# Kernel tuning notes

Hardware: AMD Instinct MI355X
Metric: run time of the kernel (lower is better)

Reference implementation:

```python
import jax, jax.numpy as jnp
import numpy as np

B, S, C, L, H = 128, 8, 120, 469, 64


def setup_inputs() -> dict:
    key = jax.random.key(0)
    kx, kk, kq, kv = jax.random.split(key, 4)
    scale = 1.0 / np.sqrt(L)
    x = jax.random.normal(kx, (B, S, C, L), dtype=jnp.float32)
    # nn.Linear(L, H, bias=False): y = x @ W^T with W:[H,L]; store as [L,H] so y = x @ W
    Wk = jax.random.normal(kk, (L, H), dtype=jnp.float32) * scale
    Wq = jax.random.normal(kq, (L, H), dtype=jnp.float32) * scale
    Wv = jax.random.normal(kv, (L, H), dtype=jnp.float32) * scale
    return {"x": x, "Wk": Wk, "Wq": Wq, "Wv": Wv}


def reference(x, Wk, Wq, Wv):
    b, s, c, l = x.shape
    h = Wk.shape[-1]
    # torch: x.view(S_, B, C_, L_) -- a raw reshape, not a permute
    xs = x.reshape(s, b, c, l)
    k = xs @ Wk  # (s, b, c, h)
    q = xs @ Wq
    v = xs @ Wv
    wei = jnp.einsum('sbch,sbdh->sbcd', q, k) * (h ** -0.5)
    wei = jax.nn.softmax(wei, axis=-1)  # dropout = identity in eval
    out = jnp.einsum('sbcd,sbdh->sbch', wei, v)  # (s, b, c, h)
    # torch: matrices.view(B, S_, C_, head_size) -- raw reshape again
    return out.reshape(b, s, c, h)
```

## Files before the change

kernel.cpp:

```cpp
#include <hip/hip_runtime.h>
#include <hip/hip_bf16.h>

typedef __attribute__((ext_vector_type(8))) short bf16x8;
typedef __attribute__((ext_vector_type(4))) float f32x4;
typedef float f32x4u __attribute__((ext_vector_type(4), aligned(4)));
typedef __attribute__((ext_vector_type(4))) short short4v;
typedef unsigned short ushort_t;

#define CC 120
#define LL 469
#define HH 64

constexpr int NBATCH = 1024;
constexpr int KSTEPS = 15;

constexpr int WB_SHORTS   = 8192;
constexpr int SMEM_BYTES  = 49152;
constexpr int WIMG_SHORTS = KSTEPS * WB_SHORTS;
constexpr int WIMG_BYTES  = WIMG_SHORTS * 2;

__device__ __forceinline__ ushort_t f2bf(float f) {
  __hip_bfloat16 h = __float2bfloat16(f);
  return __builtin_bit_cast(ushort_t, h);
}

__device__ __forceinline__ void gload_lds16(const void* g, void* l) {
  __builtin_amdgcn_global_load_lds(
      (const __attribute__((address_space(1))) unsigned int*)g,
      (__attribute__((address_space(3))) unsigned int*)l, 16, 0, 0);
}

__device__ __forceinline__ char* sptr(char* base, int row, int stride, int byteoff) {
  return base + row * stride + (byteoff ^ ((row & 7) << 4));
}

__global__ void prep_w(const float* __restrict__ Wk, const float* __restrict__ Wq,
                       const float* __restrict__ Wv, ushort_t* __restrict__ wimg) {
  int idx = blockIdx.x * 256 + threadIdx.x;
  int t = idx / WB_SHORTS;
  int r = idx % WB_SHORTS;
  int col = r / 40, kk = r % 40;
  float v = 0.f;
  if (r < 192 * 40 && kk < 32) {
    int kb = (t == 14) ? 437 : t * 32;
    int k = kb + kk;
    bool live = (k < LL) && (t < 14 || k >= 448);
    if (live) {
      int wsel = col >> 6, h = col & 63;
      const float* wp = (wsel == 0) ? Wk : (wsel == 1) ? Wq : Wv;
      v = wp[(size_t)k * HH + h];
    }
  }
  wimg[idx] = f2bf(v);
}

#define XISSUE(T, X0, X1, X2, X3)                                              \
  {                                                                            \
    const int _k = (((T) == 14) ? 437 : (T) * 32) + lg * 8;                    \
    X0 = *(const f32x4u*)(xr0 + _k);                                           \
    X1 = *(const f32x4u*)(xr0 + _k + 4);                                       \
    X2 = *(const f32x4u*)(xr1c + _k);                                          \
    X3 = *(const f32x4u*)(xr1c + _k + 4);                                      \
  }
#define WISSUE(T)                                                              \
  {                                                                            \
    const char* _src = (const char*)(wimg + (size_t)(T) * WB_SHORTS);          \
    char* _dst = (char*)(Wl + ((T) % 3) * WB_SHORTS);                          \
    _Pragma("unroll")                                                          \
    for (int _i = 0; _i < 4; ++_i) {                                           \
      int _c = wv + 4 * _i;                                                    \
      gload_lds16(_src + _c * 1024 + lane * 16, _dst + _c * 1024);             \
    }                                                                          \
  }
#define ENDREGION(N)                                                           \
  {                                                                            \
    __builtin_amdgcn_sched_barrier(0);                                         \
    asm volatile("s_waitcnt vmcnt(" #N ")" ::: "memory");                      \
    __builtin_amdgcn_sched_barrier(0);                                         \
    __builtin_amdgcn_s_barrier();                                              \
    __builtin_amdgcn_sched_barrier(0);                                         \
  }
#define COMPUTE(T, X0, X1, X2, X3)                                             \
  {                                                                            \
    const ushort_t* _wb = Wl + ((T) % 3) * WB_SHORTS;                          \
    bf16x8 _a0, _a1;                                                           \
    _Pragma("unroll")                                                          \
    for (int _j = 0; _j < 4; ++_j) {                                           \
      _a0[_j] = (short)f2bf(X0[_j]); _a0[4 + _j] = (short)f2bf(X1[_j]);        \
      _a1[_j] = (short)f2bf(X2[_j]); _a1[4 + _j] = (short)f2bf(X3[_j]);        \
    }                                                                          \
    _Pragma("unroll")                                                          \
    for (int _n = 0; _n < 12; ++_n) {                                          \
      bf16x8 _b = *(const bf16x8*)(_wb + (_n * 16 + lr) * 40 + lg * 8);        \
      acc[0][_n] = __builtin_amdgcn_mfma_f32_16x16x32_bf16(_a0, _b, acc[0][_n], 0, 0, 0); \
      acc[1][_n] = __builtin_amdgcn_mfma_f32_16x16x32_bf16(_a1, _b, acc[1][_n], 0, 0, 0); \
    }                                                                          \
  }

template <bool WIMG>
__global__ __launch_bounds__(256, 2)
void fused_regional_head(const float* __restrict__ x,
                         const float* __restrict__ Wk,
                         const float* __restrict__ Wq,
                         const float* __restrict__ Wv,
                         const ushort_t* __restrict__ wimg,
                         float* __restrict__ out) {
  __shared__ char smem[SMEM_BYTES];
  const int tid = threadIdx.x;
  const int lane = tid & 63;
  const int wv = tid >> 6;
  const int lr = lane & 15;
  const int lg = lane >> 4;
  const int batch = blockIdx.x;
  const size_t xbase = (size_t)batch * CC * LL;

  ushort_t* Wl = (ushort_t*)smem;

  const int row0 = wv * 32 + lr;
  const int row1 = wv * 32 + 16 + lr;
  const int row1c = (row1 < CC) ? row1 : (CC - 1);
  const float* xr0  = x + xbase + (size_t)row0 * LL;
  const float* xr1c = x + xbase + (size_t)row1c * LL;

  f32x4 acc[2][12];
#pragma unroll
  for (int m = 0; m < 2; ++m)
#pragma unroll
    for (int n = 0; n < 12; ++n) acc[m][n] = (f32x4){0.f, 0.f, 0.f, 0.f};

  if constexpr (WIMG) {
    f32x4u xA0, xA1, xA2, xA3, xB0, xB1, xB2, xB3, xC0, xC1, xC2, xC3;
    WISSUE(0);
    XISSUE(0, xA0, xA1, xA2, xA3);
    WISSUE(1);
    XISSUE(1, xB0, xB1, xB2, xB3);
    ENDREGION(8);
#pragma unroll
    for (int tt = 0; tt < 4; ++tt) {
      const int t = 3 * tt;
      WISSUE(t + 2); XISSUE(t + 2, xC0, xC1, xC2, xC3);
      COMPUTE(t, xA0, xA1, xA2, xA3);
      ENDREGION(8);
      WISSUE(t + 3); XISSUE(t + 3, xA0, xA1, xA2, xA3);
      COMPUTE(t + 1, xB0, xB1, xB2, xB3);
      ENDREGION(8);
      WISSUE(t + 4); XISSUE(t + 4, xB0, xB1, xB2, xB3);
      COMPUTE(t + 2, xC0, xC1, xC2, xC3);
      ENDREGION(8);
    }
    WISSUE(14); XISSUE(14, xC0, xC1, xC2, xC3);
    COMPUTE(12, xA0, xA1, xA2, xA3);
    ENDREGION(8);
    COMPUTE(13, xB0, xB1, xB2, xB3);
    ENDREGION(0);
    COMPUTE(14, xC0, xC1, xC2, xC3);
  } else {
    for (int t = 0; t < KSTEPS; ++t) {
      const int kb = (t == 14) ? 437 : t * 32;
      f32x4u x0 = *(const f32x4u*)(xr0 + kb + lg * 8);
      f32x4u x1 = *(const f32x4u*)(xr0 + kb + lg * 8 + 4);
      f32x4u x2 = *(const f32x4u*)(xr1c + kb + lg * 8);
      f32x4u x3 = *(const f32x4u*)(xr1c + kb + lg * 8 + 4);
      bf16x8 a0, a1;
#pragma unroll
      for (int j = 0; j < 4; ++j) {
        a0[j] = (short)f2bf(x0[j]); a0[4 + j] = (short)f2bf(x1[j]);
        a1[j] = (short)f2bf(x2[j]); a1[4 + j] = (short)f2bf(x3[j]);
      }
#pragma unroll
      for (int n = 0; n < 12; ++n) {
        int col = n * 16 + lr;
        int wsel = col >> 6, h = col & 63;
        const float* wp = (wsel == 0) ? Wk : (wsel == 1) ? Wq : Wv;
        bf16x8 b;
#pragma unroll
        for (int j = 0; j < 8; ++j) {
          int k = kb + lg * 8 + j;
          bool live = (k < LL) && (t < 14 || k >= 448);
          b[j] = (short)f2bf(live ? wp[(size_t)k * HH + h] : 0.f);
        }
        acc[0][n] = __builtin_amdgcn_mfma_f32_16x16x32_bf16(a0, b, acc[0][n], 0, 0, 0);
        acc[1][n] = __builtin_amdgcn_mfma_f32_16x16x32_bf16(a1, b, acc[1][n], 0, 0, 0);
      }
    }
  }
  __syncthreads();

  char* Qb = smem;
  char* Kb = smem + 16384;
  char* Vb = smem + 32768;
  char* Pb = smem;
#pragma unroll
  for (int mt = 0; mt < 2; ++mt) {
#pragma unroll
    for (int r = 0; r < 4; ++r) {
      int row = wv * 32 + mt * 16 + lg * 4 + r;
#pragma unroll
      for (int n = 0; n < 4; ++n) {
        *(ushort_t*)sptr(Kb, row, 128, (n * 16 + lr) * 2) = f2bf(acc[mt][n][r]);
        *(ushort_t*)sptr(Qb, row, 128, (n * 16 + lr) * 2) = f2bf(acc[mt][4 + n][r]);
      }
    }
#pragma unroll
    for (int n = 0; n < 4; ++n) {
      short4v pk;
#pragma unroll
      for (int r = 0; r < 4; ++r) pk[r] = (short)f2bf(acc[mt][8 + n][r]);
      *(short4v*)sptr(Vb, n * 16 + lr, 256, (wv * 32 + mt * 16 + lg * 4) * 2) = pk;
    }
  }
  __syncthreads();

  f32x4 accw[2][8];
#pragma unroll
  for (int m = 0; m < 2; ++m)
#pragma unroll
    for (int n = 0; n < 8; ++n) accw[m][n] = (f32x4){0.f, 0.f, 0.f, 0.f};
#pragma unroll
  for (int ks = 0; ks < 2; ++ks) {
    bf16x8 a0 = *(const bf16x8*)sptr(Qb, wv * 32 + lr, 128, ks * 64 + lg * 16);
    bf16x8 a1 = *(const bf16x8*)sptr(Qb, wv * 32 + 16 + lr, 128, ks * 64 + lg * 16);
#pragma unroll
    for (int n = 0; n < 8; ++n) {
      bf16x8 b = *(const bf16x8*)sptr(Kb, n * 16 + lr, 128, ks * 64 + lg * 16);
      accw[0][n] = __builtin_amdgcn_mfma_f32_16x16x32_bf16(a0, b, accw[0][n], 0, 0, 0);
      accw[1][n] = __builtin_amdgcn_mfma_f32_16x16x32_bf16(a1, b, accw[1][n], 0, 0, 0);
    }
  }
  __syncthreads();

#pragma unroll
  for (int mt = 0; mt < 2; ++mt)
#pragma unroll
    for (int r = 0; r < 4; ++r) {
      float l[8];
      float m = -1e30f;
#pragma unroll
      for (int n = 0; n < 8; ++n) {
        float v = accw[mt][n][r] * 0.125f;
        if (n == 7 && lr >= 8) v = -1e30f;
        l[n] = v;
        m = fmaxf(m, v);
      }
#pragma unroll
      for (int off = 1; off < 16; off <<= 1) m = fmaxf(m, __shfl_xor(m, off));
      float s = 0.f;
#pragma unroll
      for (int n = 0; n < 8; ++n) {
        float p = __expf(l[n] - m);
        l[n] = p;
        s += p;
      }
#pragma unroll
      for (int off = 1; off < 16; off <<= 1) s += __shfl_xor(s, off);
      float inv = 1.f / s;
      int row = wv * 32 + mt * 16 + lg * 4 + r;
#pragma unroll
      for (int n = 0; n < 8; ++n)
        *(ushort_t*)sptr(Pb, row, 256, (n * 16 + lr) * 2) = f2bf(l[n] * inv);
    }

  f32x4 acco[2][4];
#pragma unroll
  for (int m = 0; m < 2; ++m)
#pragma unroll
    for (int n = 0; n < 4; ++n) acco[m][n] = (f32x4){0.f, 0.f, 0.f, 0.f};
#pragma unroll
  for (int ks = 0; ks < 4; ++ks) {
    bf16x8 a0 = *(const bf16x8*)sptr(Pb, wv * 32 + lr, 256, ks * 64 + lg * 16);
    bf16x8 a1 = *(const bf16x8*)sptr(Pb, wv * 32 + 16 + lr, 256, ks * 64 + lg * 16);
#pragma unroll
    for (int n = 0; n < 4; ++n) {
      bf16x8 b = *(const bf16x8*)sptr(Vb, n * 16 + lr, 256, ks * 64 + lg * 16);
      acco[0][n] = __builtin_amdgcn_mfma_f32_16x16x32_bf16(a0, b, acco[0][n], 0, 0, 0);
      acco[1][n] = __builtin_amdgcn_mfma_f32_16x16x32_bf16(a1, b, acco[1][n], 0, 0, 0);
    }
  }

  __syncthreads();
  float* Ob = (float*)smem;
#pragma unroll
  for (int mt = 0; mt < 2; ++mt)
#pragma unroll
    for (int r = 0; r < 4; ++r) {
      int row = wv * 32 + mt * 16 + lg * 4 + r;
      if (row < CC) {
#pragma unroll
        for (int n = 0; n < 4; ++n)
          Ob[row * 68 + n * 16 + lr] = acco[mt][n][r];
      }
    }
  __syncthreads();
  const size_t obase = (size_t)batch * CC * HH;
#pragma unroll
  for (int i = 0; i < 8; ++i) {
    int idx = i * 256 + tid;
    if (idx < 1920) {
      int row = idx >> 4;
      int c4 = (idx & 15) * 4;
      f32x4 v = *(const f32x4*)(Ob + row * 68 + c4);
      *(f32x4*)(out + obase + (size_t)idx * 4) = v;
    }
  }
}

extern "C" void kernel_launch(void* const* d_in, const int* in_sizes, int n_in,
                              void* d_out, int out_size, void* d_ws, size_t ws_size,
                              hipStream_t stream) {
  (void)in_sizes; (void)n_in; (void)out_size;
  const float* x  = (const float*)d_in[0];
  const float* Wk = (const float*)d_in[1];
  const float* Wq = (const float*)d_in[2];
  const float* Wv = (const float*)d_in[3];
  float* out = (float*)d_out;
  if (ws_size >= (size_t)WIMG_BYTES && d_ws != nullptr) {
    ushort_t* wimg = (ushort_t*)d_ws;
    prep_w<<<480, 256, 0, stream>>>(Wk, Wq, Wv, wimg);
    fused_regional_head<true><<<NBATCH, 256, 0, stream>>>(x, Wk, Wq, Wv, wimg, out);
  } else {
    fused_regional_head<false><<<NBATCH, 256, 0, stream>>>(x, Wk, Wq, Wv, nullptr, out);
  }
}
```

Measured before the change: 68.24 us.

## Split each batch across 8 waves with one 16-row tile per wave

The fused kernel now launches 512 threads (8 waves) per block instead of 256, and each wave owns a single 16-row M tile instead of two. Per-thread accumulators, x loads and weight-tile LDS copies are halved, and wait counts are adjusted to match. The aim is more waves in flight to hide global-load latency and lower register pressure. The cost is that each LDS weight tile is now reused by only one MFMA A operand per wave, and block-wide barriers span more waves.

```diff
diff --git a/kernel.cpp b/kernel.cpp
--- a/kernel.cpp
+++ b/kernel.cpp
@@ -54,21 +54,19 @@
   wimg[idx] = f2bf(v);
 }
 
-#define XISSUE(T, X0, X1, X2, X3)                                              \
+#define XISSUE(T, X0, X1)                                                      \
   {                                                                            \
     const int _k = (((T) == 14) ? 437 : (T) * 32) + lg * 8;                    \
     X0 = *(const f32x4u*)(xr0 + _k);                                           \
     X1 = *(const f32x4u*)(xr0 + _k + 4);                                       \
-    X2 = *(const f32x4u*)(xr1c + _k);                                          \
-    X3 = *(const f32x4u*)(xr1c + _k + 4);                                      \
   }
 #define WISSUE(T)                                                              \
   {                                                                            \
     const char* _src = (const char*)(wimg + (size_t)(T) * WB_SHORTS);          \
     char* _dst = (char*)(Wl + ((T) % 3) * WB_SHORTS);                          \
     _Pragma("unroll")                                                          \
-    for (int _i = 0; _i < 4; ++_i) {                                           \
-      int _c = wv + 4 * _i;                                                    \
+    for (int _i = 0; _i < 2; ++_i) {                                           \
+      int _c = wv * 2 + _i;                                                    \
       gload_lds16(_src + _c * 1024 + lane * 16, _dst + _c * 1024);             \
     }                                                                          \
   }
@@ -80,25 +78,23 @@
     __builtin_amdgcn_s_barrier();                                              \
     __builtin_amdgcn_sched_barrier(0);                                         \
   }
-#define COMPUTE(T, X0, X1, X2, X3)                                             \
+#define COMPUTE(T, X0, X1)                                                     \
   {                                                                            \
     const ushort_t* _wb = Wl + ((T) % 3) * WB_SHORTS;                          \
-    bf16x8 _a0, _a1;                                                           \
+    bf16x8 _a0;                                                                \
     _Pragma("unroll")                                                          \
     for (int _j = 0; _j < 4; ++_j) {                                           \
       _a0[_j] = (short)f2bf(X0[_j]); _a0[4 + _j] = (short)f2bf(X1[_j]);        \
-      _a1[_j] = (short)f2bf(X2[_j]); _a1[4 + _j] = (short)f2bf(X3[_j]);        \
     }                                                                          \
     _Pragma("unroll")                                                          \
     for (int _n = 0; _n < 12; ++_n) {                                          \
       bf16x8 _b = *(const bf16x8*)(_wb + (_n * 16 + lr) * 40 + lg * 8);        \
-      acc[0][_n] = __builtin_amdgcn_mfma_f32_16x16x32_bf16(_a0, _b, acc[0][_n], 0, 0, 0); \
-      acc[1][_n] = __builtin_amdgcn_mfma_f32_16x16x32_bf16(_a1, _b, acc[1][_n], 0, 0, 0); \
+      acc[_n] = __builtin_amdgcn_mfma_f32_16x16x32_bf16(_a0, _b, acc[_n], 0, 0, 0); \
     }                                                                          \
   }
 
 template <bool WIMG>
-__global__ __launch_bounds__(256, 2)
+__global__ __launch_bounds__(512, 4)
 void fused_regional_head(const float* __restrict__ x,
                          const float* __restrict__ Wk,
                          const float* __restrict__ Wq,
@@ -116,56 +112,47 @@
 
   ushort_t* Wl = (ushort_t*)smem;
 
-  const int row0 = wv * 32 + lr;
-  const int row1 = wv * 32 + 16 + lr;
-  const int row1c = (row1 < CC) ? row1 : (CC - 1);
-  const float* xr0  = x + xbase + (size_t)row0 * LL;
-  const float* xr1c = x + xbase + (size_t)row1c * LL;
-
-  f32x4 acc[2][12];
-#pragma unroll
-  for (int m = 0; m < 2; ++m)
-#pragma unroll
-    for (int n = 0; n < 12; ++n) acc[m][n] = (f32x4){0.f, 0.f, 0.f, 0.f};
+  const int row0 = wv * 16 + lr;
+  const int row0c = (row0 < CC) ? row0 : (CC - 1);
+  const float* xr0 = x + xbase + (size_t)row0c * LL;
+
+  f32x4 acc[12];
+#pragma unroll
+  for (int n = 0; n < 12; ++n) acc[n] = (f32x4){0.f, 0.f, 0.f, 0.f};
 
   if constexpr (WIMG) {
-    f32x4u xA0, xA1, xA2, xA3, xB0, xB1, xB2, xB3, xC0, xC1, xC2, xC3;
-    WISSUE(0);
-    XISSUE(0, xA0, xA1, xA2, xA3);
-    WISSUE(1);
-    XISSUE(1, xB0, xB1, xB2, xB3);
-    ENDREGION(8);
+    f32x4u xA0, xA1, xB0, xB1, xC0, xC1;
+    WISSUE(0); XISSUE(0, xA0, xA1);
+    WISSUE(1); XISSUE(1, xB0, xB1);
+    ENDREGION(4);
 #pragma unroll
     for (int tt = 0; tt < 4; ++tt) {
       const int t = 3 * tt;
-      WISSUE(t + 2); XISSUE(t + 2, xC0, xC1, xC2, xC3);
-      COMPUTE(t, xA0, xA1, xA2, xA3);
-      ENDREGION(8);
-      WISSUE(t + 3); XISSUE(t + 3, xA0, xA1, xA2, xA3);
-      COMPUTE(t + 1, xB0, xB1, xB2, xB3);
-      ENDREGION(8);
-      WISSUE(t + 4); XISSUE(t + 4, xB0, xB1, xB2, xB3);
-      COMPUTE(t + 2, xC0, xC1, xC2, xC3);
-      ENDREGION(8);
-    }
-    WISSUE(14); XISSUE(14, xC0, xC1, xC2, xC3);
-    COMPUTE(12, xA0, xA1, xA2, xA3);
-    ENDREGION(8);
-    COMPUTE(13, xB0, xB1, xB2, xB3);
+      WISSUE(t + 2); XISSUE(t + 2, xC0, xC1);
+      COMPUTE(t, xA0, xA1);
+      ENDREGION(4);
+      WISSUE(t + 3); XISSUE(t + 3, xA0, xA1);
+      COMPUTE(t + 1, xB0, xB1);
+      ENDREGION(4);
+      WISSUE(t + 4); XISSUE(t + 4, xB0, xB1);
+      COMPUTE(t + 2, xC0, xC1);
+      ENDREGION(4);
+    }
+    WISSUE(14); XISSUE(14, xC0, xC1);
+    COMPUTE(12, xA0, xA1);
+    ENDREGION(4);
+    COMPUTE(13, xB0, xB1);
     ENDREGION(0);
-    COMPUTE(14, xC0, xC1, xC2, xC3);
+    COMPUTE(14, xC0, xC1);
   } else {
     for (int t = 0; t < KSTEPS; ++t) {
       const int kb = (t == 14) ? 437 : t * 32;
       f32x4u x0 = *(const f32x4u*)(xr0 + kb + lg * 8);
       f32x4u x1 = *(const f32x4u*)(xr0 + kb + lg * 8 + 4);
-      f32x4u x2 = *(const f32x4u*)(xr1c + kb + lg * 8);
-      f32x4u x3 = *(const f32x4u*)(xr1c + kb + lg * 8 + 4);
-      bf16x8 a0, a1;
+      bf16x8 a0;
 #pragma unroll
       for (int j = 0; j < 4; ++j) {
         a0[j] = (short)f2bf(x0[j]); a0[4 + j] = (short)f2bf(x1[j]);
-        a1[j] = (short)f2bf(x2[j]); a1[4 + j] = (short)f2bf(x3[j]);
       }
 #pragma unroll
       for (int n = 0; n < 12; ++n) {
@@ -179,8 +166,7 @@
           bool live = (k < LL) && (t < 14 || k >= 448);
           b[j] = (short)f2bf(live ? wp[(size_t)k * HH + h] : 0.f);
         }
-        acc[0][n] = __builtin_amdgcn_mfma_f32_16x16x32_bf16(a0, b, acc[0][n], 0, 0, 0);
-        acc[1][n] = __builtin_amdgcn_mfma_f32_16x16x32_bf16(a1, b, acc[1][n], 0, 0, 0);
+        acc[n] = __builtin_amdgcn_mfma_f32_16x16x32_bf16(a0, b, acc[n], 0, 0, 0);
       }
     }
   }
@@ -191,110 +177,95 @@
   char* Vb = smem + 32768;
   char* Pb = smem;
 #pragma unroll
-  for (int mt = 0; mt < 2; ++mt) {
-#pragma unroll
-    for (int r = 0; r < 4; ++r) {
-      int row = wv * 32 + mt * 16 + lg * 4 + r;
-#pragma unroll
-      for (int n = 0; n < 4; ++n) {
-        *(ushort_t*)sptr(Kb, row, 128, (n * 16 + lr) * 2) = f2bf(acc[mt][n][r]);
-        *(ushort_t*)sptr(Qb, row, 128, (n * 16 + lr) * 2) = f2bf(acc[mt][4 + n][r]);
-      }
-    }
+  for (int r = 0; r < 4; ++r) {
+    int row = wv * 16 + lg * 4 + r;
 #pragma unroll
     for (int n = 0; n < 4; ++n) {
-      short4v pk;
-#pragma unroll
-      for (int r = 0; r < 4; ++r) pk[r] = (short)f2bf(acc[mt][8 + n][r]);
-      *(short4v*)sptr(Vb, n * 16 + lr, 256, (wv * 32 + mt * 16 + lg * 4) * 2) = pk;
-    }
-  }
-  __syncthreads();
-
-  f32x4 accw[2][8];
-#pragma unroll
-  for (int m = 0; m < 2; ++m)
-#pragma unroll
-    for (int n = 0; n < 8; ++n) accw[m][n] = (f32x4){0.f, 0.f, 0.f, 0.f};
+      *(ushort_t*)sptr(Kb, row, 128, (n * 16 + lr) * 2) = f2bf(acc[n][r]);
+      *(ushort_t*)sptr(Qb, row, 128, (n * 16 + lr) * 2) = f2bf(acc[4 + n][r]);
+    }
+  }
+#pragma unroll
+  for (int n = 0; n < 4; ++n) {
+    short4v pk;
+#pragma unroll
+    for (int r = 0; r < 4; ++r) pk[r] = (short)f2bf(acc[8 + n][r]);
+    *(short4v*)sptr(Vb, n * 16 + lr, 256, (wv * 16 + lg * 4) * 2) = pk;
+  }
+  __syncthreads();
+
+  f32x4 accw[8];
+#pragma unroll
+  for (int n = 0; n < 8; ++n) accw[n] = (f32x4){0.f, 0.f, 0.f, 0.f};
 #pragma unroll
   for (int ks = 0; ks < 2; ++ks) {
-    bf16x8 a0 = *(const bf16x8*)sptr(Qb, wv * 32 + lr, 128, ks * 64 + lg * 16);
-    bf16x8 a1 = *(const bf16x8*)sptr(Qb, wv * 32 + 16 + lr, 128, ks * 64 + lg * 16);
+    bf16x8 a0 = *(const bf16x8*)sptr(Qb, wv * 16 + lr, 128, ks * 64 + lg * 16);
 #pragma unroll
     for (int n = 0; n < 8; ++n) {
       bf16x8 b = *(const bf16x8*)sptr(Kb, n * 16 + lr, 128, ks * 64 + lg * 16);
-      accw[0][n] = __builtin_amdgcn_mfma_f32_16x16x32_bf16(a0, b, accw[0][n], 0, 0, 0);
-      accw[1][n] = __builtin_amdgcn_mfma_f32_16x16x32_bf16(a1, b, accw[1][n], 0, 0, 0);
-    }
-  }
-  __syncthreads();
-
-#pragma unroll
-  for (int mt = 0; mt < 2; ++mt)
-#pragma unroll
-    for (int r = 0; r < 4; ++r) {
-      float l[8];
-      float m = -1e30f;
-#pragma unroll
-      for (int n = 0; n < 8; ++n) {
-        float v = accw[mt][n][r] * 0.125f;
-        if (n == 7 && lr >= 8) v = -1e30f;
-        l[n] = v;
-        m = fmaxf(m, v);
-      }
-#pragma unroll
-      for (int off = 1; off < 16; off <<= 1) m = fmaxf(m, __shfl_xor(m, off));
-      float s = 0.f;
-#pragma unroll
-      for (int n = 0; n < 8; ++n) {
-        float p = __expf(l[n] - m);
-        l[n] = p;
-        s += p;
-      }
-#pragma unroll
-      for (int off = 1; off < 16; off <<= 1) s += __shfl_xor(s, off);
-      float inv = 1.f / s;
-      int row = wv * 32 + mt * 16 + lg * 4 + r;
-#pragma unroll
-      for (int n = 0; n < 8; ++n)
-        *(ushort_t*)sptr(Pb, row, 256, (n * 16 + lr) * 2) = f2bf(l[n] * inv);
-    }
-
-  f32x4 acco[2][4];
-#pragma unroll
-  for (int m = 0; m < 2; ++m)
-#pragma unroll
-    for (int n = 0; n < 4; ++n) acco[m][n] = (f32x4){0.f, 0.f, 0.f, 0.f};
+      accw[n] = __builtin_amdgcn_mfma_f32_16x16x32_bf16(a0, b, accw[n], 0, 0, 0);
+    }
+  }
+  __syncthreads();
+
+#pragma unroll
+  for (int r = 0; r < 4; ++r) {
+    float l[8];
+    float m = -1e30f;
+#pragma unroll
+    for (int n = 0; n < 8; ++n) {
+      float v = accw[n][r] * 0.125f;
+      if (n == 7 && lr >= 8) v = -1e30f;
+      l[n] = v;
+      m = fmaxf(m, v);
+    }
+#pragma unroll
+    for (int off = 1; off < 16; off <<= 1) m = fmaxf(m, __shfl_xor(m, off));
+    float s = 0.f;
+#pragma unroll
+    for (int n = 0; n < 8; ++n) {
+      float p = __expf(l[n] - m);
+      l[n] = p;
+      s += p;
+    }
+#pragma unroll
+    for (int off = 1; off < 16; off <<= 1) s += __shfl_xor(s, off);
+    float inv = 1.f / s;
+    int row = wv * 16 + lg * 4 + r;
+#pragma unroll
+    for (int n = 0; n < 8; ++n)
+      *(ushort_t*)sptr(Pb, row, 256, (n * 16 + lr) * 2) = f2bf(l[n] * inv);
+  }
+
+  f32x4 acco[4];
+#pragma unroll
+  for (int n = 0; n < 4; ++n) acco[n] = (f32x4){0.f, 0.f, 0.f, 0.f};
 #pragma unroll
   for (int ks = 0; ks < 4; ++ks) {
-    bf16x8 a0 = *(const bf16x8*)sptr(Pb, wv * 32 + lr, 256, ks * 64 + lg * 16);
-    bf16x8 a1 = *(const bf16x8*)sptr(Pb, wv * 32 + 16 + lr, 256, ks * 64 + lg * 16);
+    bf16x8 a0 = *(const bf16x8*)sptr(Pb, wv * 16 + lr, 256, ks * 64 + lg * 16);
 #pragma unroll
     for (int n = 0; n < 4; ++n) {
       bf16x8 b = *(const bf16x8*)sptr(Vb, n * 16 + lr, 256, ks * 64 + lg * 16);
-      acco[0][n] = __builtin_amdgcn_mfma_f32_16x16x32_bf16(a0, b, acco[0][n], 0, 0, 0);
-      acco[1][n] = __builtin_amdgcn_mfma_f32_16x16x32_bf16(a1, b, acco[1][n], 0, 0, 0);
+      acco[n] = __builtin_amdgcn_mfma_f32_16x16x32_bf16(a0, b, acco[n], 0, 0, 0);
     }
   }
 
   __syncthreads();
   float* Ob = (float*)smem;
 #pragma unroll
-  for (int mt = 0; mt < 2; ++mt)
-#pragma unroll
-    for (int r = 0; r < 4; ++r) {
-      int row = wv * 32 + mt * 16 + lg * 4 + r;
-      if (row < CC) {
-#pragma unroll
-        for (int n = 0; n < 4; ++n)
-          Ob[row * 68 + n * 16 + lr] = acco[mt][n][r];
-      }
-    }
+  for (int r = 0; r < 4; ++r) {
+    int row = wv * 16 + lg * 4 + r;
+    if (row < CC) {
+#pragma unroll
+      for (int n = 0; n < 4; ++n)
+        Ob[row * 68 + n * 16 + lr] = acco[n][r];
+    }
+  }
   __syncthreads();
   const size_t obase = (size_t)batch * CC * HH;
 #pragma unroll
-  for (int i = 0; i < 8; ++i) {
-    int idx = i * 256 + tid;
+  for (int i = 0; i < 4; ++i) {
+    int idx = i * 512 + tid;
     if (idx < 1920) {
       int row = idx >> 4;
       int c4 = (idx & 15) * 4;
@@ -316,8 +287,8 @@
   if (ws_size >= (size_t)WIMG_BYTES && d_ws != nullptr) {
     ushort_t* wimg = (ushort_t*)d_ws;
     prep_w<<<480, 256, 0, stream>>>(Wk, Wq, Wv, wimg);
-    fused_regional_head<true><<<NBATCH, 256, 0, stream>>>(x, Wk, Wq, Wv, wimg, out);
+    fused_regional_head<true><<<NBATCH, 512, 0, stream>>>(x, Wk, Wq, Wv, wimg, out);
   } else {
-    fused_regional_head<false><<<NBATCH, 256, 0, stream>>>(x, Wk, Wq, Wv, nullptr, out);
-  }
-}
+    fused_regional_head<false><<<NBATCH, 512, 0, stream>>>(x, Wk, Wq, Wv, nullptr, out);
+  }
+}
```

Result: slower. 69.97 us (+2.5%).
